# Kernel tuning notes

Hardware: AMD Instinct MI355X
Metric: run time of the kernel (lower is better)

Reference implementation:

```python
import jax, jax.numpy as jnp
import numpy as np


def _conv(x, w, b):
    # x: [N,Cin,H,W], w: [Cout,Cin,kh,kw]
    y = jax.lax.conv_general_dilated(x, w, (1, 1), 'SAME',
                                     dimension_numbers=('NCHW', 'OIHW', 'NCHW'))
    return y + b[None, :, None, None]


def _up2(x):
    n, c, h, w = x.shape
    return jax.image.resize(x, (n, c, 2 * h, 2 * w), method='bilinear')


def setup_inputs() -> dict:
    key = jax.random.key(0)
    ks = jax.random.split(key, 24)
    N, C, H, W = 4, 256, 128, 128
    D, L, NUM_CLASSES = 512, 8, 75
    f32 = jnp.float32

    def rn(k, shape, scale=0.02):
        return jax.random.normal(k, shape, dtype=f32) * scale

    inp = {
        'p2': jax.random.normal(ks[0], (N, C, H, W), dtype=f32),
        'p3': jax.random.normal(ks[1], (N, C, H // 2, W // 2), dtype=f32),
        'p4': jax.random.normal(ks[2], (N, C, H // 4, W // 4), dtype=f32),
        'p5': jax.random.normal(ks[3], (N, C, H // 8, W // 8), dtype=f32),
        'rel_coord': jax.random.normal(ks[4], (N, 2, H, W), dtype=f32),
        'abs_coord': jax.random.normal(ks[5], (N, 2, H, W), dtype=f32),
        'fg_mask': jax.random.randint(ks[6], (N, 1, H, W), 0, 2, dtype=jnp.int32),
    }
    # scale-head convs: p2 x1 (no up), p3 x1 (+up), p4 x2 (+up each), p5 x3 (+up each)
    for i, nm in enumerate(['w_p2_0', 'w_p3_0', 'w_p4_0', 'w_p4_1', 'w_p5_0', 'w_p5_1', 'w_p5_2']):
        inp[nm] = rn(ks[7 + i], (C, C, 3, 3))
        inp['b' + nm[1:]] = jnp.zeros((C,), f32)
    # comb_pe_conv: (conv_dims + pe_dim) -> conv_dims, 3x3
    inp['comb_w'] = rn(ks[14], (C, C + 4, 3, 3))
    inp['comb_b'] = jnp.zeros((C,), f32)
    # densepose sparse head: 8 stacked submanifold 3x3 convs, dim 512
    inp['head_w0'] = rn(ks[15], (D, C, 3, 3))
    inp['head_b0'] = jnp.zeros((D,), f32)
    inp['head_w'] = rn(ks[16], (L - 1, D, D, 3, 3))
    inp['head_b'] = jnp.zeros((L - 1, D), f32)
    # predictor: 1x1 conv to num_classes
    inp['pred_w'] = rn(ks[17], (NUM_CLASSES, D, 1, 1))
    inp['pred_b'] = jnp.zeros((NUM_CLASSES,), f32)
    return inp


def reference(p2, p3, p4, p5, rel_coord, abs_coord, fg_mask,
              w_p2_0, b_p2_0, w_p3_0, b_p3_0, w_p4_0, b_p4_0, w_p4_1, b_p4_1,
              w_p5_0, b_p5_0, w_p5_1, b_p5_1, w_p5_2, b_p5_2,
              comb_w, comb_b, head_w0, head_b0, head_w, head_b, pred_w, pred_b):
    relu = jax.nn.relu
    # FPN scale heads merged to common stride
    x = relu(_conv(p2, w_p2_0, b_p2_0))
    x = x + _up2(relu(_conv(p3, w_p3_0, b_p3_0)))
    t = _up2(relu(_conv(p4, w_p4_0, b_p4_0)))
    x = x + _up2(relu(_conv(t, w_p4_1, b_p4_1)))
    t = _up2(relu(_conv(p5, w_p5_0, b_p5_0)))
    t = _up2(relu(_conv(t, w_p5_1, b_p5_1)))
    x = x + _up2(relu(_conv(t, w_p5_2, b_p5_2)))
    # concat positional encodings, comb conv
    x = jnp.concatenate([x, rel_coord, abs_coord], axis=1)  # [N, C+4, H, W]
    x = relu(_conv(x, comb_w, comb_b))
    # sparse gather -> submanifold sparse conv head -> dense scatter.
    # Masking inputs and outputs at each layer is math-equivalent to spconv's
    # SparseConvTensor built from fg_mask-active coords, SubM convs, then .dense().
    mask = (fg_mask > 0).astype(x.dtype)  # [N,1,H,W]
    h = x * mask
    h = relu(_conv(h, head_w0, head_b0)) * mask
    for i in range(head_w.shape[0]):
        h = relu(_conv(h, head_w[i], head_b[i])) * mask
    # dense predictor (1x1 conv) on scattered dense tensor
    return _conv(h, pred_w, pred_b)  # [N, 75, H, W]
```

## Files before the change

kernel.cpp:

```cpp
#include <hip/hip_runtime.h>
#include <cstdint>
#include <cstddef>

#define THREADS 256

typedef _Float16 f16x8 __attribute__((ext_vector_type(8)));
typedef _Float16 f16x4 __attribute__((ext_vector_type(4)));
typedef _Float16 f16x2 __attribute__((ext_vector_type(2)));
typedef float f32x4 __attribute__((ext_vector_type(4)));
typedef float f32x8 __attribute__((ext_vector_type(8)));

__device__ __forceinline__ void gll16(const void* g, void* l) {
    __builtin_amdgcn_global_load_lds(
        (const __attribute__((address_space(1))) unsigned int*)g,
        (__attribute__((address_space(3))) unsigned int*)l, 16, 0, 0);
}

__global__ void pack_scale_all_kernel(
    const float* __restrict__ w0, const float* __restrict__ w1,
    const float* __restrict__ w2, const float* __restrict__ w3,
    const float* __restrict__ w4, const float* __restrict__ w5,
    const float* __restrict__ w6, const float* __restrict__ w7,
    _Float16* __restrict__ wp)
{
    const int wi = blockIdx.y;
    const float* w = (wi == 0) ? w0 : (wi == 1) ? w1 : (wi == 2) ? w2 : (wi == 3) ? w3
                   : (wi == 4) ? w4 : (wi == 5) ? w5 : (wi == 6) ? w6 : w7;
    const int Cin = (wi == 7) ? 260 : 256;
    const int CC  = (wi == 7) ? 9 : 8;
    _Float16* dst = wp + (size_t)wi * 663552;
    int idx = blockIdx.x * THREADS + threadIdx.x;
    int total = 256 * CC * 4;
    if (idx >= total) return;
    int u = idx & 3;
    int cc = (idx >> 2) % CC;
    int co = (idx >> 2) / CC;
    int ci0 = cc * 32 + u * 8;
    for (int tap = 0; tap < 9; ++tap) {
        f16x8 v;
#pragma unroll
        for (int j = 0; j < 8; ++j) {
            int ci = ci0 + j;
            v[j] = (ci < Cin) ? (_Float16)w[((size_t)co * Cin + ci) * 9 + tap] : (_Float16)0.f;
        }
        *reinterpret_cast<f16x8*>(dst + ((((size_t)tap * CC + cc) * 4 + u) * 256 + co) * 8) = v;
    }
}

__global__ void pack_whead_all_kernel(const float* __restrict__ hw0,
                                      const float* __restrict__ hw,
                                      _Float16* __restrict__ wp0,
                                      _Float16* __restrict__ wpH)
{
    const int wi = blockIdx.y;
    const int Cin = (wi == 0) ? 256 : 512;
    const float* w = (wi == 0) ? hw0 : hw + (size_t)(wi - 1) * 2359296;
    _Float16* wp = (wi == 0) ? wp0 : wpH + (size_t)(wi - 1) * 2359296;
    const int NSTEP = 9 * (Cin / 64);
    int idx = blockIdx.x * THREADS + threadIdx.x;
    int total = 512 * NSTEP * 8;
    if (idx >= total) return;
    int kc = idx & 7;
    int t = (idx >> 3) % NSTEP;
    int co = (idx >> 3) / NSTEP;
    int gy = co >> 8;
    int r = co & 255;
    int kcs = kc ^ (r & 7);
    int k = t * 64 + kcs * 8;
    int tap = k / Cin;
    int cib = k - tap * Cin;
    f16x8 v;
#pragma unroll
    for (int j = 0; j < 8; ++j)
        v[j] = (_Float16)w[((size_t)co * Cin + cib + j) * 9 + tap];
    *reinterpret_cast<f16x8*>(wp + ((size_t)(t * 2 + gy) * 2048 + r * 8 + kc) * 8) = v;
}

__global__ void zerows_kernel(float* __restrict__ p)
{
    p[blockIdx.x * THREADS + threadIdx.x] = 0.f;
}

__global__ void zero2_kernel(_Float16* __restrict__ a, _Float16* __restrict__ b)
{
    const size_t N = 4ull * 16384 * 512;
    for (size_t i = ((size_t)blockIdx.x * THREADS + threadIdx.x) * 8; i < N;
         i += (size_t)gridDim.x * THREADS * 8) {
        *reinterpret_cast<f16x8*>(a + i) = (f16x8){};
        *reinterpret_cast<f16x8*>(b + i) = (f16x8){};
    }
}

__global__ __launch_bounds__(1024)
void compact_kernel(const int* __restrict__ fg, int* __restrict__ list)
{
    __shared__ int part[1024];
    const int tid = threadIdx.x;
    const int base = tid * 64;
    int cnt = 0;
    for (int j = 0; j < 64; ++j) cnt += (fg[base + j] > 0) ? 1 : 0;
    part[tid] = cnt;
    __syncthreads();
    for (int off = 1; off < 1024; off <<= 1) {
        int v = (tid >= off) ? part[tid - off] : 0;
        __syncthreads();
        part[tid] += v;
        __syncthreads();
    }
    int pos = part[tid] - cnt;
    for (int j = 0; j < 64; ++j)
        if (fg[base + j] > 0) list[pos++] = base + j;
    const int total = part[1023];
    for (int i = total + tid; i < 40960; i += 1024) list[i] = -1;
}

__global__ __launch_bounds__(256)
void t_all_kernel(const float* __restrict__ s2, const float* __restrict__ s3,
                  const float* __restrict__ s4, const float* __restrict__ s5,
                  _Float16* __restrict__ d2, _Float16* __restrict__ d3,
                  _Float16* __restrict__ d4, _Float16* __restrict__ d5)
{
    __shared__ _Float16 tile[64 * 32];
    const int lvl = blockIdx.z >> 2;
    const int n = blockIdx.z & 3;
    const int HW = 16384 >> (2 * lvl);
    const int p0 = blockIdx.x * 64;
    if (p0 >= HW) return;
    const float* in = (lvl == 0) ? s2 : (lvl == 1) ? s3 : (lvl == 2) ? s4 : s5;
    _Float16* out = (lvl == 0) ? d2 : (lvl == 1) ? d3 : (lvl == 2) ? d4 : d5;
    const int C = 256;
    const int c0 = blockIdx.y * 32;
    const int tid = threadIdx.x;
    {
        int ci = tid >> 3;
        int j8 = (tid & 7) * 8;
        f32x8 v = *reinterpret_cast<const f32x8*>(in + ((size_t)n * C + c0 + ci) * HW + p0 + j8);
#pragma unroll
        for (int j = 0; j < 8; ++j)
            tile[(j8 + j) * 32 + ci] = (_Float16)v[j];
    }
    __syncthreads();
    {
        int px = tid >> 2;
        int u = tid & 3;
        f16x8 v = *reinterpret_cast<const f16x8*>(&tile[px * 32 + u * 8]);
        *reinterpret_cast<f16x8*>(out + ((size_t)n * HW + p0 + px) * C + c0 + u * 8) = v;
    }
}

template<int INF32, int OUTMODE, int CC>
__global__ __launch_bounds__(512, 4)
void convu_kernel(const void* __restrict__ inv, const _Float16* __restrict__ wp,
                  const float* __restrict__ bias, const int* __restrict__ msk,
                  void* __restrict__ outp, int Cout, int H, int W,
                  int inCst, int outCst, int useMask)
{
    __shared__ _Float16 Xs[2 * 1344 * 8];

    const int tid = threadIdx.x;
    const int lane = tid & 63;
    const int wave = tid >> 6;
    const int lm = lane & 15;
    const int lu = lane >> 4;
    const int waveco = (wave & 1) * 64;
    const int wrow = (wave >> 1) * 4;
    const int n = blockIdx.z;
    const int co0 = blockIdx.y * 128;
    const int tpr = W >> 4;
    const int tx = blockIdx.x % tpr;
    const int ty = blockIdx.x / tpr;
    const int x0 = tx << 4;
    const int y0 = ty << 4;
    const int HW = H * W;

    int soff[3];
#pragma unroll
    for (int t = 0; t < 3; ++t) {
        int s = tid + t * 512;
        int item = s >> 2, u = s & 3;
        int row = item / 18, col = item - row * 18;
        int y = y0 + row - 1, x = x0 + col - 1;
        soff[t] = (s < 1296 && y >= 0 && y < H && x >= 0 && x < W)
                      ? ((n * HW + y * W + x) * inCst + u * 8) : -1;
    }

    f32x4 acc[4][4];
#pragma unroll
    for (int m = 0; m < 4; ++m)
#pragma unroll
        for (int nf = 0; nf < 4; ++nf)
            acc[m][nf] = (f32x4){0.f, 0.f, 0.f, 0.f};

    const size_t tstride = (size_t)CC * 4 * Cout * 8;
    f32x8 rr[3];

    if (INF32 == 0) {
        const _Float16* src = (const _Float16*)inv;
#pragma unroll
        for (int t = 0; t < 3; ++t) {
            int s = tid + t * 512;
            if (s < 1296 && soff[t] < 0) {
                *reinterpret_cast<f16x8*>(&Xs[s * 8]) = (f16x8){};
                *reinterpret_cast<f16x8*>(&Xs[(1344 + s) * 8]) = (f16x8){};
            }
        }
#pragma unroll
        for (int t = 0; t < 3; ++t) {
            int s = tid + t * 512;
            if (s < 1296 && soff[t] >= 0)
                gll16(src + soff[t], &Xs[(t * 512 + (tid & ~63)) * 8]);
        }
    } else {
        const float* srcf = (const float*)inv;
#pragma unroll
        for (int t = 0; t < 3; ++t) {
            int s = tid + t * 512;
            rr[t] = (f32x8){};
            if (s < 1296 && soff[t] >= 0)
                rr[t] = *reinterpret_cast<const f32x8*>(srcf + soff[t]);
        }
#pragma unroll
        for (int t = 0; t < 3; ++t) {
            int s = tid + t * 512;
            if (s < 1296) {
                f16x8 h;
#pragma unroll
                for (int j = 0; j < 8; ++j) h[j] = (_Float16)rr[t][j];
                *reinterpret_cast<f16x8*>(&Xs[s * 8]) = h;
            }
        }
    }
    __syncthreads();

    int bsel = 0;
    for (int cc = 0; cc < CC; ++cc) {
        if (cc + 1 < CC) {
            if (INF32 == 0) {
                const _Float16* src = (const _Float16*)inv;
#pragma unroll
                for (int t = 0; t < 3; ++t) {
                    int s = tid + t * 512;
                    if (s < 1296 && soff[t] >= 0)
                        gll16(src + soff[t] + (cc + 1) * 32,
                              &Xs[((bsel ^ 1) * 1344 + t * 512 + (tid & ~63)) * 8]);
                }
            } else {
                const float* srcf = (const float*)inv;
#pragma unroll
                for (int t = 0; t < 3; ++t) {
                    int s = tid + t * 512;
                    rr[t] = (f32x8){};
                    if (s < 1296 && soff[t] >= 0)
                        rr[t] = *reinterpret_cast<const f32x8*>(srcf + soff[t] + (cc + 1) * 32);
                }
            }
        }
        {
            const int xbase = bsel * 1344;
            const _Float16* wb = wp + (((size_t)cc * 4 + lu) * Cout + co0 + waveco + lm) * 8;
#pragma unroll
            for (int tap = 0; tap < 9; ++tap) {
                const int dy = tap / 3, dx = tap % 3;
                const _Float16* wt = wb + (size_t)tap * tstride;
                f16x8 a[4], b[4];
#pragma unroll
                for (int m = 0; m < 4; ++m)
                    a[m] = *reinterpret_cast<const f16x8*>(wt + m * 128);
#pragma unroll
                for (int nf = 0; nf < 4; ++nf) {
                    int slot = ((wrow + nf + dy) * 18 + lm + dx) * 4 + lu;
                    b[nf] = *reinterpret_cast<const f16x8*>(&Xs[(xbase + slot) * 8]);
                }
#pragma unroll
                for (int m = 0; m < 4; ++m)
#pragma unroll
                    for (int nf = 0; nf < 4; ++nf)
                        acc[m][nf] = __builtin_amdgcn_mfma_f32_16x16x32_f16(a[m], b[nf], acc[m][nf], 0, 0, 0);
            }
        }
        if (INF32 == 1 && cc + 1 < CC) {
#pragma unroll
            for (int t = 0; t < 3; ++t) {
                int s = tid + t * 512;
                if (s < 1296) {
                    f16x8 h;
#pragma unroll
                    for (int j = 0; j < 8; ++j) h[j] = (_Float16)rr[t][j];
                    *reinterpret_cast<f16x8*>(&Xs[((bsel ^ 1) * 1344 + s) * 8]) = h;
                }
            }
        }
        __syncthreads();
        bsel ^= 1;
    }

    const int xE = x0 + lm;
    const size_t nHW = (size_t)n * HW;
#pragma unroll
    for (int nf = 0; nf < 4; ++nf) {
        const int y = y0 + wrow + nf;
        float mv = 1.f;
        if (useMask) mv = (msk[nHW + y * W + xE] > 0) ? 1.f : 0.f;
        const size_t pixo = (nHW + (size_t)y * W + xE) * outCst;
#pragma unroll
        for (int m = 0; m < 4; ++m) {
            const int cb = co0 + waveco + m * 16 + lu * 4;
            const f32x4 bv = *reinterpret_cast<const f32x4*>(bias + cb);
            if (OUTMODE == 0) {
                f16x4 h;
#pragma unroll
                for (int r = 0; r < 4; ++r)
                    h[r] = (_Float16)(fmaxf(acc[m][nf][r] + bv[r], 0.f) * mv);
                *reinterpret_cast<f16x4*>((_Float16*)outp + pixo + cb) = h;
            } else if (OUTMODE == 1) {
                f32x4 v;
#pragma unroll
                for (int r = 0; r < 4; ++r)
                    v[r] = fmaxf(acc[m][nf][r] + bv[r], 0.f);
                *reinterpret_cast<f32x4*>((float*)outp + pixo + cb) = v;
            } else {
                f32x4 old = *reinterpret_cast<const f32x4*>((float*)outp + pixo + cb);
#pragma unroll
                for (int r = 0; r < 4; ++r)
                    old[r] += fmaxf(acc[m][nf][r] + bv[r], 0.f);
                *reinterpret_cast<f32x4*>((float*)outp + pixo + cb) = old;
            }
        }
    }
}

template<int CIN>
__global__ __launch_bounds__(512, 1)
void gemm_head_kernel(const _Float16* __restrict__ in,
                      const _Float16* __restrict__ wpk,
                      const float* __restrict__ bias,
                      const int* __restrict__ list,
                      _Float16* __restrict__ outp,
                      const _Float16* __restrict__ zpage)
{
    constexpr int SPT = CIN / 64;
    __shared__ __attribute__((aligned(16))) char ldsb[2 * 73728];

    const int job = blockIdx.x;
    const int xcd = job & 7;
    const int r8 = job >> 3;
    const int tile = xcd * 16 + (r8 >> 1);
    const int gy = r8 & 1;
    if (list[tile * 320] < 0) return;

    const int tid = threadIdx.x;
    const int lane = tid & 63;
    const int wave = tid >> 6;
    const int lm = lane & 15;
    const int lu = lane >> 4;
    const int wco = (wave & 1) * 128;
    const int g80 = (wave >> 1) * 80;
    const int co0 = gy * 256;

    const _Float16* bptr[5];
    unsigned long long inbm = 0;
    int dstA[4], dstB[5];
#pragma unroll
    for (int s = 0; s < 5; ++s) {
        const int row = s * 64 + (tid >> 3);
        const int kc = (tid & 7) ^ (row & 7);
        const int entry = list[tile * 320 + row];
        bptr[s] = zpage;
        if (entry >= 0) {
            const int y = (entry >> 7) & 127;
            const int x = entry & 127;
            bptr[s] = in + (size_t)entry * CIN + kc * 8;
#pragma unroll
            for (int tap = 0; tap < 9; ++tap) {
                const int yy = y + tap / 3 - 1;
                const int xx = x + tap % 3 - 1;
                if ((unsigned)yy < 128u && (unsigned)xx < 128u)
                    inbm |= 1ull << (s * 9 + tap);
            }
        }
        dstB[s] = 32768 + (s * 512 + (tid & ~63)) * 16;
    }
#pragma unroll
    for (int s = 0; s < 4; ++s) dstA[s] = (s * 512 + (tid & ~63)) * 16;

    auto STAGE = [&](int t, int bufByte) {
        const _Float16* as = wpk + (size_t)(t * 2 + gy) * 16384;
#pragma unroll
        for (int s = 0; s < 4; ++s)
            gll16(as + (size_t)(s * 512 + tid) * 8, ldsb + bufByte + dstA[s]);
        const int tap = t / SPT;
        const int ci0 = (t % SPT) * 64;
        const int delta = ((tap / 3 - 1) * 128 + (tap % 3 - 1)) * CIN + ci0;
#pragma unroll
        for (int s = 0; s < 5; ++s) {
            const bool ok = (inbm >> (s * 9 + tap)) & 1ull;
            const _Float16* src = ok ? (bptr[s] + delta) : zpage;
            gll16(src, ldsb + bufByte + dstB[s]);
        }
    };

    f32x4 acc[8][5];
#pragma unroll
    for (int m = 0; m < 8; ++m)
#pragma unroll
        for (int n = 0; n < 5; ++n)
            acc[m][n] = (f32x4){0.f, 0.f, 0.f, 0.f};

    STAGE(0, 0);
    __syncthreads();

    int bsel = 0;
    for (int cb = 0; cb < SPT; ++cb) {
        for (int tap = 0; tap < 9; ++tap) {
            if (tap < 8) STAGE((tap + 1) * SPT + cb, (bsel ^ 1) * 73728);
            else if (cb + 1 < SPT) STAGE(cb + 1, (bsel ^ 1) * 73728);
            const int ab = bsel * 73728;
#pragma unroll
            for (int s = 0; s < 2; ++s) {
                f16x8 bfr[5];
#pragma unroll
                for (int n = 0; n < 5; ++n) {
                    const int row = g80 + n * 16 + lm;
                    const int ch = (s * 4 + lu) ^ (row & 7);
                    bfr[n] = *reinterpret_cast<const f16x8*>(ldsb + ab + 32768 + row * 128 + ch * 16);
                }
#pragma unroll
                for (int m = 0; m < 8; ++m) {
                    const int row = wco + m * 16 + lm;
                    const int ch = (s * 4 + lu) ^ (row & 7);
                    const f16x8 afr = *reinterpret_cast<const f16x8*>(ldsb + ab + row * 128 + ch * 16);
#pragma unroll
                    for (int n = 0; n < 5; ++n)
                        acc[m][n] = __builtin_amdgcn_mfma_f32_16x16x32_f16(afr, bfr[n], acc[m][n], 0, 0, 0);
                }
            }
            __syncthreads();
            bsel ^= 1;
        }
    }

#pragma unroll
    for (int n = 0; n < 5; ++n) {
        const int entry = list[tile * 320 + g80 + n * 16 + lm];
        if (entry < 0) continue;
        _Float16* pp = outp + (size_t)entry * 512 + co0 + wco;
#pragma unroll
        for (int m = 0; m < 8; ++m) {
            const f32x4 bv = *reinterpret_cast<const f32x4*>(bias + co0 + wco + m * 16 + lu * 4);
            f16x4 h;
#pragma unroll
            for (int rr = 0; rr < 4; ++rr)
                h[rr] = (_Float16)fmaxf(acc[m][n][rr] + bv[rr], 0.f);
            *reinterpret_cast<f16x4*>(pp + m * 16 + lu * 4) = h;
        }
    }
}

__global__ void up2h_kernel(const _Float16* __restrict__ in, _Float16* __restrict__ out,
                            int Hin, int Win)
{
    const int Wout = Win << 1, Hout = Hin << 1;
    const int lw = __ffs(Wout) - 1, lh = __ffs(Hout) - 1;
    int i = blockIdx.x * THREADS + threadIdx.x;
    if (i >= 4 * Hout * Wout * 32) return;
    int u = i & 31;
    int p = i >> 5;
    int x = p & (Wout - 1);
    int y = (p >> lw) & (Hout - 1);
    int n = p >> (lw + lh);
    int iy = y >> 1, ix = x >> 1;
    int y2 = (y & 1) ? min(iy + 1, Hin - 1) : max(iy - 1, 0);
    int x2 = (x & 1) ? min(ix + 1, Win - 1) : max(ix - 1, 0);
    const _Float16* base = in + ((size_t)n * Hin * Win) * 256 + u * 8;
    f16x8 v00 = *reinterpret_cast<const f16x8*>(base + (iy * Win + ix) * 256);
    f16x8 v01 = *reinterpret_cast<const f16x8*>(base + (iy * Win + x2) * 256);
    f16x8 v10 = *reinterpret_cast<const f16x8*>(base + (y2 * Win + ix) * 256);
    f16x8 v11 = *reinterpret_cast<const f16x8*>(base + (y2 * Win + x2) * 256);
    f16x8 o;
#pragma unroll
    for (int j = 0; j < 8; ++j) {
        float v = 0.5625f * (float)v00[j] + 0.1875f * ((float)v01[j] + (float)v10[j])
                + 0.0625f * (float)v11[j];
        o[j] = (_Float16)v;
    }
    *reinterpret_cast<f16x8*>(out + (((size_t)n * Hout * Wout) + y * Wout + x) * 256 + u * 8) = o;
}

__global__ void up2addh_kernel(const float* __restrict__ in, _Float16* __restrict__ Xch)
{
    int i = blockIdx.x * THREADS + threadIdx.x;
    if (i >= 4 * 16384 * 32) return;
    int u = i & 31;
    int p = i >> 5;
    int x = p & 127;
    int y = (p >> 7) & 127;
    int n = p >> 14;
    int iy = y >> 1, ix = x >> 1;
    int y2 = (y & 1) ? min(iy + 1, 63) : max(iy - 1, 0);
    int x2 = (x & 1) ? min(ix + 1, 63) : max(ix - 1, 0);
    const float* base = in + ((size_t)n * 4096) * 256 + u * 8;
    f32x8 v00 = *reinterpret_cast<const f32x8*>(base + (iy * 64 + ix) * 256);
    f32x8 v01 = *reinterpret_cast<const f32x8*>(base + (iy * 64 + x2) * 256);
    f32x8 v10 = *reinterpret_cast<const f32x8*>(base + (y2 * 64 + ix) * 256);
    f32x8 v11 = *reinterpret_cast<const f32x8*>(base + (y2 * 64 + x2) * 256);
    _Float16* dst = Xch + ((size_t)n * 16384 + y * 128 + x) * 288 + u * 8;
    f16x8 d = *reinterpret_cast<const f16x8*>(dst);
#pragma unroll
    for (int j = 0; j < 8; ++j)
        d[j] = (_Float16)((float)d[j] + 0.5625f * v00[j]
               + 0.1875f * (v01[j] + v10[j]) + 0.0625f * v11[j]);
    *reinterpret_cast<f16x8*>(dst) = d;
}

__global__ void coords2h_kernel(const float* __restrict__ rel, const float* __restrict__ abs_,
                                _Float16* __restrict__ Xch)
{
    int i = blockIdx.x * THREADS + threadIdx.x;
    if (i >= 4 * 16384) return;
    int px = i & 16383;
    int n = i >> 14;
    _Float16* dst = Xch + ((size_t)n * 16384 + px) * 288 + 256;
    f16x8 v0 = (f16x8){};
    v0[0] = (_Float16)rel[((size_t)n * 2 + 0) * 16384 + px];
    v0[1] = (_Float16)rel[((size_t)n * 2 + 1) * 16384 + px];
    v0[2] = (_Float16)abs_[((size_t)n * 2 + 0) * 16384 + px];
    v0[3] = (_Float16)abs_[((size_t)n * 2 + 1) * 16384 + px];
    *reinterpret_cast<f16x8*>(dst) = v0;
    *reinterpret_cast<f16x8*>(dst + 8) = (f16x8){};
    *reinterpret_cast<f16x8*>(dst + 16) = (f16x8){};
    *reinterpret_cast<f16x8*>(dst + 24) = (f16x8){};
}

__global__ __launch_bounds__(256)
void predh_kernel(const _Float16* __restrict__ in, const float* __restrict__ w,
                  const float* __restrict__ bias, float* __restrict__ out)
{
    __shared__ _Float16 lw[25 * 512];
    const int co0 = blockIdx.y * 25;
    const int n = blockIdx.z;
    for (int idx = threadIdx.x; idx < 25 * 512; idx += 256)
        lw[idx] = (_Float16)w[(size_t)(co0 + idx / 512) * 512 + (idx & 511)];
    __syncthreads();
    int px = blockIdx.x * 256 + threadIdx.x;
    const _Float16* ip = in + ((size_t)n * 16384 + px) * 512;
    float acc[25];
#pragma unroll
    for (int j = 0; j < 25; ++j) acc[j] = bias[co0 + j];
    for (int g = 0; g < 64; ++g) {
        union { f16x8 v; f16x2 p[4]; } xv;
        xv.v = *reinterpret_cast<const f16x8*>(ip + g * 8);
#pragma unroll
        for (int j = 0; j < 25; ++j) {
            union { f16x8 v; f16x2 p[4]; } wv;
            wv.v = *reinterpret_cast<const f16x8*>(&lw[j * 512 + g * 8]);
#if __has_builtin(__builtin_amdgcn_fdot2)
#pragma unroll
            for (int k = 0; k < 4; ++k)
                acc[j] = __builtin_amdgcn_fdot2(xv.p[k], wv.p[k], acc[j], false);
#else
#pragma unroll
            for (int k = 0; k < 8; ++k)
                acc[j] = fmaf((float)xv.v[k], (float)wv.v[k], acc[j]);
#endif
        }
    }
    float* op = out + ((size_t)n * 75) * 16384 + px;
#pragma unroll
    for (int j = 0; j < 25; ++j)
        op[(size_t)(co0 + j) * 16384] = acc[j];
}

extern "C" void kernel_launch(void* const* d_in, const int* in_sizes, int n_in,
                              void* d_out, int out_size, void* d_ws, size_t ws_size,
                              hipStream_t stream)
{
    const float* p2   = (const float*)d_in[0];
    const float* p3   = (const float*)d_in[1];
    const float* p4   = (const float*)d_in[2];
    const float* p5   = (const float*)d_in[3];
    const float* rel  = (const float*)d_in[4];
    const float* abs_ = (const float*)d_in[5];
    const int*   fg   = (const int*)d_in[6];
    const float* w_p2_0 = (const float*)d_in[7];
    const float* b_p2_0 = (const float*)d_in[8];
    const float* w_p3_0 = (const float*)d_in[9];
    const float* b_p3_0 = (const float*)d_in[10];
    const float* w_p4_0 = (const float*)d_in[11];
    const float* b_p4_0 = (const float*)d_in[12];
    const float* w_p4_1 = (const float*)d_in[13];
    const float* b_p4_1 = (const float*)d_in[14];
    const float* w_p5_0 = (const float*)d_in[15];
    const float* b_p5_0 = (const float*)d_in[16];
    const float* w_p5_1 = (const float*)d_in[17];
    const float* b_p5_1 = (const float*)d_in[18];
    const float* w_p5_2 = (const float*)d_in[19];
    const float* b_p5_2 = (const float*)d_in[20];
    const float* comb_w = (const float*)d_in[21];
    const float* comb_b = (const float*)d_in[22];
    const float* head_w0 = (const float*)d_in[23];
    const float* head_b0 = (const float*)d_in[24];
    const float* head_w  = (const float*)d_in[25];
    const float* head_b  = (const float*)d_in[26];
    const float* pred_w  = (const float*)d_in[27];
    const float* pred_b  = (const float*)d_in[28];

    float* ws = (float*)d_ws;
    _Float16* Xch     = (_Float16*)ws;
    _Float16* pingA   = (_Float16*)ws;
    _Float16* pingB   = (_Float16*)(ws + 18874368);
    float*    regD    = ws + 35651584;
    _Float16* p2h     = (_Float16*)regD;
    _Float16* combOut = (_Float16*)regD;
    float*    t64sum  = regD;
    _Float16* t64b    = (_Float16*)(regD + 4194304);
    _Float16* t64c    = (_Float16*)(regD + 5242880);
    _Float16* t32a    = (_Float16*)(regD + 6291456);
    _Float16* t32b    = (_Float16*)(regD + 6553600);
    _Float16* t32c    = (_Float16*)(regD + 6815744);
    _Float16* t16a    = (_Float16*)(regD + 7077888);
    _Float16* p3h     = (_Float16*)(ws + 44040192);
    _Float16* p4h     = (_Float16*)(ws + 46137344);
    _Float16* p5h     = (_Float16*)(ws + 46661632);
    _Float16* wpScale = (_Float16*)(ws + 46792704);
    float*    zpage   = ws + 49446912;
    _Float16* wpH0    = (_Float16*)(ws + 49447936);
    _Float16* wpH     = (_Float16*)(ws + 50037760);
    int*      actList = (int*)(ws + 58295296);

    auto wpS = [&](int i) { return wpScale + (size_t)i * 663552; };

    auto convu = [&](const void* in, const _Float16* wpk, const float* bs, void* outp,
                     int mode, int Cout, int H, int W,
                     int inCst, int outCst, int useMask) {
        dim3 grid((W / 16) * (H / 16), Cout / 128, 4);
        dim3 blk(512);
        if (mode == 0)
            convu_kernel<0, 0, 8><<<grid, blk, 0, stream>>>(in, wpk, bs, fg, outp, Cout, H, W, inCst, outCst, useMask);
        else if (mode == 1)
            convu_kernel<0, 1, 8><<<grid, blk, 0, stream>>>(in, wpk, bs, fg, outp, Cout, H, W, inCst, outCst, useMask);
        else if (mode == 2)
            convu_kernel<0, 2, 8><<<grid, blk, 0, stream>>>(in, wpk, bs, fg, outp, Cout, H, W, inCst, outCst, useMask);
        else
            convu_kernel<0, 0, 9><<<grid, blk, 0, stream>>>(in, wpk, bs, fg, outp, Cout, H, W, inCst, outCst, useMask);
    };
    auto up2h = [&](const _Float16* in, _Float16* out, int Hin, int Win) {
        int total = 4 * (Hin * 2) * (Win * 2) * 32;
        up2h_kernel<<<dim3((total + THREADS - 1) / THREADS), dim3(THREADS), 0, stream>>>(
            in, out, Hin, Win);
    };

    zerows_kernel<<<dim3(4), dim3(THREADS), 0, stream>>>(zpage);
    compact_kernel<<<dim3(1), dim3(1024), 0, stream>>>(fg, actList);
    pack_scale_all_kernel<<<dim3(36, 8), dim3(THREADS), 0, stream>>>(
        w_p2_0, w_p3_0, w_p4_0, w_p4_1, w_p5_0, w_p5_1, w_p5_2, comb_w, wpScale);
    pack_whead_all_kernel<<<dim3(1152, 8), dim3(THREADS), 0, stream>>>(
        head_w0, head_w, wpH0, wpH);
    t_all_kernel<<<dim3(256, 8, 16), dim3(256), 0, stream>>>(
        p2, p3, p4, p5, p2h, p3h, p4h, p5h);

    convu(p2h, wpS(0), b_p2_0, Xch, 0, 256, 128, 128, 256, 288, 0);
    coords2h_kernel<<<dim3(256), dim3(THREADS), 0, stream>>>(rel, abs_, Xch);

    convu(p3h, wpS(1), b_p3_0, t64sum, 1, 256, 64, 64, 256, 256, 0);

    convu(p4h, wpS(2), b_p4_0, t32a, 0, 256, 32, 32, 256, 256, 0);
    up2h(t32a, t64b, 32, 32);
    convu(t64b, wpS(3), b_p4_1, t64sum, 2, 256, 64, 64, 256, 256, 0);

    convu(p5h, wpS(4), b_p5_0, t16a, 0, 256, 16, 16, 256, 256, 0);
    up2h(t16a, t32b, 16, 16);
    convu(t32b, wpS(5), b_p5_1, t32c, 0, 256, 32, 32, 256, 256, 0);
    up2h(t32c, t64c, 32, 32);
    convu(t64c, wpS(6), b_p5_2, t64sum, 2, 256, 64, 64, 256, 256, 0);

    up2addh_kernel<<<dim3(8192), dim3(THREADS), 0, stream>>>(t64sum, Xch);

    convu(Xch, wpS(7), comb_b, combOut, 3, 256, 128, 128, 288, 256, 1);

    zero2_kernel<<<dim3(4096), dim3(THREADS), 0, stream>>>(pingA, pingB);

    gemm_head_kernel<256><<<dim3(256), dim3(512), 0, stream>>>(
        combOut, wpH0, head_b0, actList, pingA, (const _Float16*)zpage);
    {
        const _Float16* s = pingA;
        _Float16* d = pingB;
        for (int i = 0; i < 7; ++i) {
            gemm_head_kernel<512><<<dim3(256), dim3(512), 0, stream>>>(
                s, wpH + (size_t)i * 2359296, head_b + (size_t)i * 512, actList, d,
                (const _Float16*)zpage);
            _Float16* tmp = (_Float16*)s; s = d; d = tmp;
        }
    }

    predh_kernel<<<dim3(64, 3, 4), dim3(256), 0, stream>>>(pingB, pred_w, pred_b, (float*)d_out);
}
```

Measured before the change: 2.366 ms.

## Replace full-resolution p2 and comb convs with dense implicit-GEMM kernel

Adds a gemm_dense_kernel that runs a 3x3 conv as an implicit GEMM. Each block computes a 256-output-channel by 256-pixel tile with 8x4 MFMA fragments per wave, staged through double-buffered, XOR-swizzled LDS via global_load_lds, with a zero page standing in for padded taps. The two 128x128 convs (p2 and comb) now use it, and the concat buffer stride grows from 288 to 320 so the comb conv's input channels are a multiple of 64. The aim is better operand reuse and fewer syncs than the previous 128-channel convu tiles, at the cost of one block per CU and extra padding work on the 320-channel input.

```diff
diff --git a/kernel.cpp b/kernel.cpp
--- a/kernel.cpp
+++ b/kernel.cpp
@@ -45,6 +45,28 @@
         }
         *reinterpret_cast<f16x8*>(dst + ((((size_t)tap * CC + cc) * 4 + u) * 256 + co) * 8) = v;
     }
+}
+
+__global__ void pack_wdense_kernel(const float* __restrict__ w, _Float16* __restrict__ wp,
+                                   int CinTrue, int CINP)
+{
+    const int NSTEP = 9 * (CINP / 64);
+    int idx = blockIdx.x * THREADS + threadIdx.x;
+    if (idx >= 256 * NSTEP * 8) return;
+    int kc = idx & 7;
+    int t = (idx >> 3) % NSTEP;
+    int co = (idx >> 3) / NSTEP;
+    int kcs = kc ^ (co & 7);
+    int k = t * 64 + kcs * 8;
+    int tap = k / CINP;
+    int cib = k - tap * CINP;
+    f16x8 v;
+#pragma unroll
+    for (int j = 0; j < 8; ++j) {
+        int ci = cib + j;
+        v[j] = (ci < CinTrue) ? (_Float16)w[((size_t)co * CinTrue + ci) * 9 + tap] : (_Float16)0.f;
+    }
+    *reinterpret_cast<f16x8*>(wp + ((size_t)t * 2048 + co * 8 + kc) * 8) = v;
 }
 
 __global__ void pack_whead_all_kernel(const float* __restrict__ hw0,
@@ -192,9 +214,8 @@
             acc[m][nf] = (f32x4){0.f, 0.f, 0.f, 0.f};
 
     const size_t tstride = (size_t)CC * 4 * Cout * 8;
-    f32x8 rr[3];
-
-    if (INF32 == 0) {
+
+    {
         const _Float16* src = (const _Float16*)inv;
 #pragma unroll
         for (int t = 0; t < 3; ++t) {
@@ -210,49 +231,19 @@
             if (s < 1296 && soff[t] >= 0)
                 gll16(src + soff[t], &Xs[(t * 512 + (tid & ~63)) * 8]);
         }
-    } else {
-        const float* srcf = (const float*)inv;
-#pragma unroll
-        for (int t = 0; t < 3; ++t) {
-            int s = tid + t * 512;
-            rr[t] = (f32x8){};
-            if (s < 1296 && soff[t] >= 0)
-                rr[t] = *reinterpret_cast<const f32x8*>(srcf + soff[t]);
-        }
-#pragma unroll
-        for (int t = 0; t < 3; ++t) {
-            int s = tid + t * 512;
-            if (s < 1296) {
-                f16x8 h;
-#pragma unroll
-                for (int j = 0; j < 8; ++j) h[j] = (_Float16)rr[t][j];
-                *reinterpret_cast<f16x8*>(&Xs[s * 8]) = h;
-            }
-        }
     }
     __syncthreads();
 
     int bsel = 0;
     for (int cc = 0; cc < CC; ++cc) {
         if (cc + 1 < CC) {
-            if (INF32 == 0) {
-                const _Float16* src = (const _Float16*)inv;
-#pragma unroll
-                for (int t = 0; t < 3; ++t) {
-                    int s = tid + t * 512;
-                    if (s < 1296 && soff[t] >= 0)
-                        gll16(src + soff[t] + (cc + 1) * 32,
-                              &Xs[((bsel ^ 1) * 1344 + t * 512 + (tid & ~63)) * 8]);
-                }
-            } else {
-                const float* srcf = (const float*)inv;
-#pragma unroll
-                for (int t = 0; t < 3; ++t) {
-                    int s = tid + t * 512;
-                    rr[t] = (f32x8){};
-                    if (s < 1296 && soff[t] >= 0)
-                        rr[t] = *reinterpret_cast<const f32x8*>(srcf + soff[t] + (cc + 1) * 32);
-                }
+            const _Float16* src = (const _Float16*)inv;
+#pragma unroll
+            for (int t = 0; t < 3; ++t) {
+                int s = tid + t * 512;
+                if (s < 1296 && soff[t] >= 0)
+                    gll16(src + soff[t] + (cc + 1) * 32,
+                          &Xs[((bsel ^ 1) * 1344 + t * 512 + (tid & ~63)) * 8]);
             }
         }
         {
@@ -276,18 +267,6 @@
 #pragma unroll
                     for (int nf = 0; nf < 4; ++nf)
                         acc[m][nf] = __builtin_amdgcn_mfma_f32_16x16x32_f16(a[m], b[nf], acc[m][nf], 0, 0, 0);
-            }
-        }
-        if (INF32 == 1 && cc + 1 < CC) {
-#pragma unroll
-            for (int t = 0; t < 3; ++t) {
-                int s = tid + t * 512;
-                if (s < 1296) {
-                    f16x8 h;
-#pragma unroll
-                    for (int j = 0; j < 8; ++j) h[j] = (_Float16)rr[t][j];
-                    *reinterpret_cast<f16x8*>(&Xs[((bsel ^ 1) * 1344 + s) * 8]) = h;
-                }
             }
         }
         __syncthreads();
@@ -325,6 +304,133 @@
                     old[r] += fmaxf(acc[m][nf][r] + bv[r], 0.f);
                 *reinterpret_cast<f32x4*>((float*)outp + pixo + cb) = old;
             }
+        }
+    }
+}
+
+template<int CINP, int MASK>
+__global__ __launch_bounds__(512, 1)
+void gemm_dense_kernel(const _Float16* __restrict__ in,
+                       const _Float16* __restrict__ wpk,
+                       const float* __restrict__ bias,
+                       const int* __restrict__ fg,
+                       _Float16* __restrict__ outp, int outCst,
+                       const _Float16* __restrict__ zpage)
+{
+    constexpr int SPT = CINP / 64;
+    __shared__ __attribute__((aligned(16))) char ldsb[2 * 65536];
+
+    const int job = blockIdx.x;
+    const int xcd = job & 7;
+    const int idx = job >> 3;
+    const int img = idx >> 3;
+    const int tile = xcd * 8 + (idx & 7);
+    const int x0 = (tile & 7) << 4;
+    const int y0 = (tile >> 3) << 4;
+
+    const int tid = threadIdx.x;
+    const int lane = tid & 63;
+    const int wave = tid >> 6;
+    const int lm = lane & 15;
+    const int lu = lane >> 4;
+    const int wco = (wave & 1) * 128;
+    const int wpx = (wave >> 1) * 64;
+
+    const _Float16* bsrc = in + (size_t)img * 16384 * CINP;
+
+    const _Float16* bptr[4];
+    unsigned long long inbm = 0;
+    int dstA[4], dstB[4];
+#pragma unroll
+    for (int s = 0; s < 4; ++s) {
+        const int row = s * 64 + (tid >> 3);
+        const int kc = (tid & 7) ^ (row & 7);
+        const int y = y0 + (row >> 4);
+        const int x = x0 + (row & 15);
+        bptr[s] = bsrc + (size_t)(y * 128 + x) * CINP + kc * 8;
+#pragma unroll
+        for (int tap = 0; tap < 9; ++tap) {
+            const int yy = y + tap / 3 - 1;
+            const int xx = x + tap % 3 - 1;
+            if ((unsigned)yy < 128u && (unsigned)xx < 128u)
+                inbm |= 1ull << (s * 9 + tap);
+        }
+        dstA[s] = (s * 512 + (tid & ~63)) * 16;
+        dstB[s] = 32768 + (s * 512 + (tid & ~63)) * 16;
+    }
+
+    auto STAGE = [&](int t, int bufByte) {
+        const _Float16* as = wpk + (size_t)t * 16384;
+#pragma unroll
+        for (int s = 0; s < 4; ++s)
+            gll16(as + (size_t)(s * 512 + tid) * 8, ldsb + bufByte + dstA[s]);
+        const int tap = t / SPT;
+        const int ci0 = (t % SPT) * 64;
+        const int delta = ((tap / 3 - 1) * 128 + (tap % 3 - 1)) * CINP + ci0;
+#pragma unroll
+        for (int s = 0; s < 4; ++s) {
+            const bool ok = (inbm >> (s * 9 + tap)) & 1ull;
+            const _Float16* src = ok ? (bptr[s] + delta) : zpage;
+            gll16(src, ldsb + bufByte + dstB[s]);
+        }
+    };
+
+    f32x4 acc[8][4];
+#pragma unroll
+    for (int m = 0; m < 8; ++m)
+#pragma unroll
+        for (int n = 0; n < 4; ++n)
+            acc[m][n] = (f32x4){0.f, 0.f, 0.f, 0.f};
+
+    STAGE(0, 0);
+    __syncthreads();
+
+    int bsel = 0;
+    for (int cb = 0; cb < SPT; ++cb) {
+        for (int tap = 0; tap < 9; ++tap) {
+            if (tap < 8) STAGE((tap + 1) * SPT + cb, (bsel ^ 1) * 65536);
+            else if (cb + 1 < SPT) STAGE(cb + 1, (bsel ^ 1) * 65536);
+            const int ab = bsel * 65536;
+#pragma unroll
+            for (int s = 0; s < 2; ++s) {
+                f16x8 bfr[4];
+#pragma unroll
+                for (int n = 0; n < 4; ++n) {
+                    const int row = wpx + n * 16 + lm;
+                    const int ch = (s * 4 + lu) ^ (row & 7);
+                    bfr[n] = *reinterpret_cast<const f16x8*>(ldsb + ab + 32768 + row * 128 + ch * 16);
+                }
+#pragma unroll
+                for (int m = 0; m < 8; ++m) {
+                    const int row = wco + m * 16 + lm;
+                    const int ch = (s * 4 + lu) ^ (row & 7);
+                    const f16x8 afr = *reinterpret_cast<const f16x8*>(ldsb + ab + row * 128 + ch * 16);
+#pragma unroll
+                    for (int n = 0; n < 4; ++n)
+                        acc[m][n] = __builtin_amdgcn_mfma_f32_16x16x32_f16(afr, bfr[n], acc[m][n], 0, 0, 0);
+                }
+            }
+            __syncthreads();
+            bsel ^= 1;
+        }
+    }
+
+    const int base = img * 16384;
+#pragma unroll
+    for (int n = 0; n < 4; ++n) {
+        const int px = wpx + n * 16 + lm;
+        const int y = y0 + (px >> 4), x = x0 + (px & 15);
+        float mv = 1.f;
+        if (MASK) mv = (fg[base + y * 128 + x] > 0) ? 1.f : 0.f;
+        _Float16* pp = outp + ((size_t)base + y * 128 + x) * outCst + wco;
+#pragma unroll
+        for (int m = 0; m < 8; ++m) {
+            const f32x4 bv = *reinterpret_cast<const f32x4*>(bias + wco + m * 16 + lu * 4);
+            f16x4 h;
+#pragma unroll
+            for (int rr = 0; rr < 4; ++rr)
+                h[rr] = (_Float16)(fmaxf(acc[m][n][rr] + bv[rr], 0.f) * mv);
+            *reinterpret_cast<f16x4*>(pp + m * 16 + lu * 4) = h;
         }
     }
 }
@@ -503,7 +609,7 @@
     f32x8 v01 = *reinterpret_cast<const f32x8*>(base + (iy * 64 + x2) * 256);
     f32x8 v10 = *reinterpret_cast<const f32x8*>(base + (y2 * 64 + ix) * 256);
     f32x8 v11 = *reinterpret_cast<const f32x8*>(base + (y2 * 64 + x2) * 256);
-    _Float16* dst = Xch + ((size_t)n * 16384 + y * 128 + x) * 288 + u * 8;
+    _Float16* dst = Xch + ((size_t)n * 16384 + y * 128 + x) * 320 + u * 8;
     f16x8 d = *reinterpret_cast<const f16x8*>(dst);
 #pragma unroll
     for (int j = 0; j < 8; ++j)
@@ -519,16 +625,16 @@
     if (i >= 4 * 16384) return;
     int px = i & 16383;
     int n = i >> 14;
-    _Float16* dst = Xch + ((size_t)n * 16384 + px) * 288 + 256;
+    _Float16* dst = Xch + ((size_t)n * 16384 + px) * 320 + 256;
     f16x8 v0 = (f16x8){};
     v0[0] = (_Float16)rel[((size_t)n * 2 + 0) * 16384 + px];
     v0[1] = (_Float16)rel[((size_t)n * 2 + 1) * 16384 + px];
     v0[2] = (_Float16)abs_[((size_t)n * 2 + 0) * 16384 + px];
     v0[3] = (_Float16)abs_[((size_t)n * 2 + 1) * 16384 + px];
     *reinterpret_cast<f16x8*>(dst) = v0;
-    *reinterpret_cast<f16x8*>(dst + 8) = (f16x8){};
-    *reinterpret_cast<f16x8*>(dst + 16) = (f16x8){};
-    *reinterpret_cast<f16x8*>(dst + 24) = (f16x8){};
+#pragma unroll
+    for (int b = 1; b < 8; ++b)
+        *reinterpret_cast<f16x8*>(dst + b * 8) = (f16x8){};
 }
 
 __global__ __launch_bounds__(256)
@@ -626,22 +732,22 @@
     _Float16* wpH0    = (_Float16*)(ws + 49447936);
     _Float16* wpH     = (_Float16*)(ws + 50037760);
     int*      actList = (int*)(ws + 58295296);
+    _Float16* wpComb  = (_Float16*)(ws + 58336256);
+    _Float16* wpDp2   = wpScale;
 
     auto wpS = [&](int i) { return wpScale + (size_t)i * 663552; };
 
     auto convu = [&](const void* in, const _Float16* wpk, const float* bs, void* outp,
                      int mode, int Cout, int H, int W,
-                     int inCst, int outCst, int useMask) {
+                     int inCst, int outCst) {
         dim3 grid((W / 16) * (H / 16), Cout / 128, 4);
         dim3 blk(512);
         if (mode == 0)
-            convu_kernel<0, 0, 8><<<grid, blk, 0, stream>>>(in, wpk, bs, fg, outp, Cout, H, W, inCst, outCst, useMask);
+            convu_kernel<0, 0, 8><<<grid, blk, 0, stream>>>(in, wpk, bs, fg, outp, Cout, H, W, inCst, outCst, 0);
         else if (mode == 1)
-            convu_kernel<0, 1, 8><<<grid, blk, 0, stream>>>(in, wpk, bs, fg, outp, Cout, H, W, inCst, outCst, useMask);
-        else if (mode == 2)
-            convu_kernel<0, 2, 8><<<grid, blk, 0, stream>>>(in, wpk, bs, fg, outp, Cout, H, W, inCst, outCst, useMask);
+            convu_kernel<0, 1, 8><<<grid, blk, 0, stream>>>(in, wpk, bs, fg, outp, Cout, H, W, inCst, outCst, 0);
         else
-            convu_kernel<0, 0, 9><<<grid, blk, 0, stream>>>(in, wpk, bs, fg, outp, Cout, H, W, inCst, outCst, useMask);
+            convu_kernel<0, 2, 8><<<grid, blk, 0, stream>>>(in, wpk, bs, fg, outp, Cout, H, W, inCst, outCst, 0);
     };
     auto up2h = [&](const _Float16* in, _Float16* out, int Hin, int Win) {
         int total = 4 * (Hin * 2) * (Win * 2) * 32;
@@ -653,29 +759,33 @@
     compact_kernel<<<dim3(1), dim3(1024), 0, stream>>>(fg, actList);
     pack_scale_all_kernel<<<dim3(36, 8), dim3(THREADS), 0, stream>>>(
         w_p2_0, w_p3_0, w_p4_0, w_p4_1, w_p5_0, w_p5_1, w_p5_2, comb_w, wpScale);
+    pack_wdense_kernel<<<dim3(288), dim3(THREADS), 0, stream>>>(w_p2_0, wpDp2, 256, 256);
+    pack_wdense_kernel<<<dim3(360), dim3(THREADS), 0, stream>>>(comb_w, wpComb, 260, 320);
     pack_whead_all_kernel<<<dim3(1152, 8), dim3(THREADS), 0, stream>>>(
         head_w0, head_w, wpH0, wpH);
     t_all_kernel<<<dim3(256, 8, 16), dim3(256), 0, stream>>>(
         p2, p3, p4, p5, p2h, p3h, p4h, p5h);
 
-    convu(p2h, wpS(0), b_p2_0, Xch, 0, 256, 128, 128, 256, 288, 0);
+    gemm_dense_kernel<256, 0><<<dim3(256), dim3(512), 0, stream>>>(
+        p2h, wpDp2, b_p2_0, fg, Xch, 320, (const _Float16*)zpage);
     coords2h_kernel<<<dim3(256), dim3(THREADS), 0, stream>>>(rel, abs_, Xch);
 
-    convu(p3h, wpS(1), b_p3_0, t64sum, 1, 256, 64, 64, 256, 256, 0);
-
-    convu(p4h, wpS(2), b_p4_0, t32a, 0, 256, 32, 32, 256, 256, 0);
+    convu(p3h, wpS(1), b_p3_0, t64sum, 1, 256, 64, 64, 256, 256);
+
+    convu(p4h, wpS(2), b_p4_0, t32a, 0, 256, 32, 32, 256, 256);
     up2h(t32a, t64b, 32, 32);
-    convu(t64b, wpS(3), b_p4_1, t64sum, 2, 256, 64, 64, 256, 256, 0);
-
-    convu(p5h, wpS(4), b_p5_0, t16a, 0, 256, 16, 16, 256, 256, 0);
+    convu(t64b, wpS(3), b_p4_1, t64sum, 2, 256, 64, 64, 256, 256);
+
+    convu(p5h, wpS(4), b_p5_0, t16a, 0, 256, 16, 16, 256, 256);
     up2h(t16a, t32b, 16, 16);
-    convu(t32b, wpS(5), b_p5_1, t32c, 0, 256, 32, 32, 256, 256, 0);
+    convu(t32b, wpS(5), b_p5_1, t32c, 0, 256, 32, 32, 256, 256);
     up2h(t32c, t64c, 32, 32);
-    convu(t64c, wpS(6), b_p5_2, t64sum, 2, 256, 64, 64, 256, 256, 0);
+    convu(t64c, wpS(6), b_p5_2, t64sum, 2, 256, 64, 64, 256, 256);
 
     up2addh_kernel<<<dim3(8192), dim3(THREADS), 0, stream>>>(t64sum, Xch);
 
-    convu(Xch, wpS(7), comb_b, combOut, 3, 256, 128, 128, 288, 256, 1);
+    gemm_dense_kernel<320, 1><<<dim3(256), dim3(512), 0, stream>>>(
+        Xch, wpComb, comb_b, fg, combOut, 256, (const _Float16*)zpage);
 
     zero2_kernel<<<dim3(4096), dim3(THREADS), 0, stream>>>(pingA, pingB);
 
```

New measurement: 2.212 ms, median of 7. 1.07x faster.
